# Kernel optimization log

Measured on AMD Instinct MI355X. Metric: run time of the kernel, lower is better.

Reference implementation:

```python
import jax, jax.numpy as jnp
import numpy as np

FEATURE_DIM = 128
HIDDEN_DIM = 64
MAPPING_SIZE = 64
SCALE = 10.0
B, N, H, W = 8, 65536, 56, 56


def setup_inputs() -> dict:
    key = jax.random.key(0)
    ks = jax.random.split(key, 12)
    features = jax.random.normal(ks[0], (B, FEATURE_DIM, H, W), dtype=jnp.float32)
    # points in [-1, 1]^3
    points = jax.random.uniform(ks[1], (B, N, 3), dtype=jnp.float32, minval=-1.0, maxval=1.0)
    # realistic pinhole intrinsics for a 56x56 feature map
    k_mat = jnp.array([[56.0, 0.0, 28.0], [0.0, 56.0, 28.0], [0.0, 0.0, 1.0]], dtype=jnp.float32)
    k = jnp.broadcast_to(k_mat, (B, 3, 3))
    # extrinsics: identity rotation, translate z by 2 so points are in front of camera
    rt_mat = jnp.concatenate([jnp.eye(3, dtype=jnp.float32), jnp.array([[0.0], [0.0], [2.0]], dtype=jnp.float32)], axis=1)
    rt = jnp.broadcast_to(rt_mat, (B, 3, 4))
    # learned params
    B_gauss = jax.random.normal(ks[2], (MAPPING_SIZE, 3), dtype=jnp.float32) * SCALE
    input_dim = FEATURE_DIM + 2 * MAPPING_SIZE
    W1 = jax.random.normal(ks[3], (input_dim, HIDDEN_DIM), dtype=jnp.float32) * 0.05
    b1 = jnp.zeros((HIDDEN_DIM,), dtype=jnp.float32)
    W2 = jax.random.normal(ks[4], (HIDDEN_DIM, HIDDEN_DIM), dtype=jnp.float32) * 0.05
    b2 = jnp.zeros((HIDDEN_DIM,), dtype=jnp.float32)
    W3 = jax.random.normal(ks[5], (HIDDEN_DIM, HIDDEN_DIM), dtype=jnp.float32) * 0.05
    b3 = jnp.zeros((HIDDEN_DIM,), dtype=jnp.float32)
    W4 = jax.random.normal(ks[6], (HIDDEN_DIM, 1), dtype=jnp.float32) * 0.05
    b4 = jnp.zeros((1,), dtype=jnp.float32)
    return {"features": features, "points": points, "k": k, "rt": rt,
            "B_gauss": B_gauss, "W1": W1, "b1": b1, "W2": W2, "b2": b2,
            "W3": W3, "b3": b3, "W4": W4, "b4": b4}


def _grid_sample_bilinear_zeros(grid, x, y):
    # grid: (B, C, H, W); x, y: (B, N) pixel coords (align_corners=False already unnormalized)
    Bc, C, Hc, Wc = grid.shape
    g = jnp.transpose(grid, (0, 2, 3, 1))  # (B, H, W, C)
    x0 = jnp.floor(x)
    y0 = jnp.floor(y)
    wx1 = x - x0  # frac
    wy1 = y - y0
    wx0 = 1.0 - wx1
    wy0 = 1.0 - wy1
    x0i = x0.astype(jnp.int32)
    y0i = y0.astype(jnp.int32)
    bidx = jnp.arange(Bc, dtype=jnp.int32)[:, None]  # (B, 1)

    def gather(ix, iy):
        inb = ((ix >= 0) & (ix < Wc) & (iy >= 0) & (iy < Hc)).astype(grid.dtype)  # (B, N)
        vals = g[bidx, jnp.clip(iy, 0, Hc - 1), jnp.clip(ix, 0, Wc - 1)]  # (B, N, C)
        return vals * inb[..., None]

    out = (gather(x0i, y0i) * (wx0 * wy0)[..., None]
           + gather(x0i + 1, y0i) * (wx1 * wy0)[..., None]
           + gather(x0i, y0i + 1) * (wx0 * wy1)[..., None]
           + gather(x0i + 1, y0i + 1) * (wx1 * wy1)[..., None])
    return out  # (B, N, C)


def reference(features, points, k, rt, B_gauss, W1, b1, W2, b2, W3, b3, W4, b4):
    Bc, Nc, _ = points.shape
    Hc, Wc = features.shape[-2:]
    # --- camera projection ---
    homo = jnp.concatenate([points, jnp.ones((Bc, Nc, 1), dtype=points.dtype)], axis=2)  # (B,N,4)
    cam = jnp.einsum('bij,bnj->bni', rt, homo)   # (B,N,3)
    img = jnp.einsum('bij,bnj->bni', k, cam)     # (B,N,3)
    z = img[:, :, 2:3] + 1e-8
    uv = img[:, :, :2] / z
    valid = (img[:, :, 2:3] > 0).astype(points.dtype)  # (B,N,1)
    u_norm = (2.0 * uv[..., 0] + 1.0) / Wc - 1.0
    v_norm = (2.0 * uv[..., 1] + 1.0) / Hc - 1.0
    # grid_sample align_corners=False unnormalization: ix = ((g+1)*W - 1)/2
    x = ((u_norm + 1.0) * Wc - 1.0) * 0.5
    y = ((v_norm + 1.0) * Hc - 1.0) * 0.5
    img_feats = _grid_sample_bilinear_zeros(features, x, y) * valid  # (B,N,C)
    # --- Fourier mapping ---
    x_proj = (2.0 * np.pi) * jnp.einsum('bnd,md->bnm', points, B_gauss)  # (B,N,M)
    coord_feats = jnp.concatenate([jnp.sin(x_proj), jnp.cos(x_proj)], axis=-1)  # (B,N,2M)
    # --- MLP ---
    inp = jnp.concatenate([img_feats, coord_feats], axis=2)  # (B,N,C+2M)
    h = jax.nn.relu(inp @ W1 + b1)
    h = jax.nn.relu(h @ W2 + b2)
    h = jax.nn.relu(h @ W3 + b3)
    out = h @ W4 + b4  # (B,N,1)
    return out
```

## Files before the change

### kernel.cpp

```cpp
#include <hip/hip_runtime.h>

#define FDIM 128
#define HDIM 64
#define MSIZE 64
#define IMG_W 56
#define IMG_H 56
#define NPIX (IMG_W * IMG_H)
#define NB 8
#define NPTS 65536

typedef _Float16 f16x8 __attribute__((ext_vector_type(8)));
typedef __fp16 hf16x2 __attribute__((ext_vector_type(2)));
typedef float f32x4 __attribute__((ext_vector_type(4)));

#define W2_OFF 16384
#define W3_OFF 20480
#define BG_OFF 49152
#define FT_BYTE_OFF 50176
#define TR16_BLOCKS (NPIX / 16 * NB)

__device__ __forceinline__ void lds_fence() {
    __asm__ volatile("s_waitcnt lgkmcnt(0)" ::: "memory");
}

__global__ __launch_bounds__(256) void prep_kernel(const float* __restrict__ in,
                                                   const float* __restrict__ W1,
                                                   const float* __restrict__ W2,
                                                   const float* __restrict__ W3,
                                                   const float* __restrict__ Bg,
                                                   _Float16* __restrict__ ws) {
    if (blockIdx.x < TR16_BLOCKS) {
        __shared__ float tile[16][133];
        _Float16* out = ws + FT_BYTE_OFF / 2;
        const int b = blockIdx.x / (NPIX / 16);
        const int pbase = (blockIdx.x % (NPIX / 16)) * 16;
        const int t = threadIdx.x;
        const float* src = in + (size_t)b * FDIM * NPIX;
        _Float16*    dst = out + (size_t)b * NPIX * FDIM;
        const int pq = t & 3;
        const int ch = t >> 2;
#pragma unroll
        for (int it = 0; it < 2; ++it) {
            const int c = it * 64 + ch;
            const float4 v = *(const float4*)(src + (size_t)c * NPIX + pbase + pq * 4);
            tile[pq * 4 + 0][c] = v.x;
            tile[pq * 4 + 1][c] = v.y;
            tile[pq * 4 + 2][c] = v.z;
            tile[pq * 4 + 3][c] = v.w;
        }
        __syncthreads();
        const int px = t >> 4;
        const int hk = (t & 15) * 8;
        union { f16x8 v; hf16x2 h[4]; } hv;
#pragma unroll
        for (int j = 0; j < 4; ++j)
            hv.h[j] = __builtin_amdgcn_cvt_pkrtz(tile[px][hk + 2 * j], tile[px][hk + 2 * j + 1]);
        *(f16x8*)(dst + (size_t)(pbase + px) * FDIM + hk) = hv.v;
    } else if (blockIdx.x < TR16_BLOCKS + 12) {
        const int t = (blockIdx.x - TR16_BLOCKS) * 256 + threadIdx.x;
        const int l = t & 63;
        const int q = l >> 4;
        const int col = l & 15;
        const int frag = t >> 6;
        if (frag < 32) {
            const int kt = frag >> 2, nt = frag & 3;
#pragma unroll
            for (int j = 0; j < 8; ++j) {
                int k = kt * 32 + q * 8 + j;
                int row = (k < 128) ? k : (128 + (k & 1) * 64 + ((k - 128) >> 1));
                ws[((size_t)(frag * 64 + l)) * 8 + j] = (_Float16)W1[row * HDIM + nt * 16 + col];
            }
        } else if (frag < 40) {
            const int f2 = frag - 32;
            const int kt = f2 >> 2, nt = f2 & 3;
#pragma unroll
            for (int j = 0; j < 8; ++j) {
                int row = kt * 32 + q * 8 + j;
                ws[W2_OFF + ((size_t)(f2 * 64 + l)) * 8 + j] = (_Float16)W2[row * HDIM + nt * 16 + col];
            }
        } else {
            const int f3 = frag - 40;
            const int kt = f3 >> 2, nt = f3 & 3;
#pragma unroll
            for (int j = 0; j < 8; ++j) {
                int row = kt * 32 + q * 8 + j;
                ws[W3_OFF + ((size_t)(f3 * 64 + l)) * 8 + j] = (_Float16)W3[row * HDIM + nt * 16 + col];
            }
        }
    } else {
        const int t = threadIdx.x;
        if (t < MSIZE) {
            float* bgs = (float*)((char*)ws + BG_OFF);
            bgs[t]       = Bg[t * 3 + 0];
            bgs[64 + t]  = Bg[t * 3 + 1];
            bgs[128 + t] = Bg[t * 3 + 2];
        }
    }
}

struct Rec {
    float w0[2], w1[2], w2[2], w3[2];
    int   i0[2], i1[2], i2[2], i3[2];
    float qx[2], qy[2], qz[2];
};
struct Pref {
    f16x8 a00, a10, a01, a11;
    f16x8 e00, e10, e01, e11;
};

__device__ __forceinline__ Pref pre_issue(const _Float16* __restrict__ ft,
                                          const Rec& R, int q) {
    Pref P;
    const int co0 = q * 8;
    P.a00 = *(const f16x8*)(ft + R.i0[0] + co0);
    P.a10 = *(const f16x8*)(ft + R.i1[0] + co0);
    P.a01 = *(const f16x8*)(ft + R.i2[0] + co0);
    P.a11 = *(const f16x8*)(ft + R.i3[0] + co0);
    const int co1 = 32 + q * 8;
    P.e00 = *(const f16x8*)(ft + R.i0[0] + co1);
    P.e10 = *(const f16x8*)(ft + R.i1[0] + co1);
    P.e01 = *(const f16x8*)(ft + R.i2[0] + co1);
    P.e11 = *(const f16x8*)(ft + R.i3[0] + co1);
    return P;
}

__device__ __forceinline__ void phaseF(f32x4 acc[2][4], const _Float16* __restrict__ w1l,
                                       const float* __restrict__ bgs, const Rec& R,
                                       int q, int l) {
#pragma unroll
    for (int ktf = 0; ktf < 4; ++ktf) {
        const f32x4 bgx = *(const f32x4*)(bgs + ktf * 16 + q * 4);
        const f32x4 bgy = *(const f32x4*)(bgs + 64 + ktf * 16 + q * 4);
        const f32x4 bgz = *(const f32x4*)(bgs + 128 + ktf * 16 + q * 4);
        f16x8 bf[4];
#pragma unroll
        for (int nt = 0; nt < 4; ++nt)
            bf[nt] = *(const f16x8*)(w1l + ((size_t)(((4 + ktf) * 4 + nt) * 64 + l)) * 8);
#pragma unroll
        for (int mt = 0; mt < 2; ++mt) {
            union { f16x8 v; hf16x2 h[4]; } af;
#pragma unroll
            for (int i = 0; i < 4; ++i) {
                float t = bgx[i] * R.qx[mt] + bgy[i] * R.qy[mt] + bgz[i] * R.qz[mt];
                float tf = __builtin_amdgcn_fractf(t);
                af.h[i] = __builtin_amdgcn_cvt_pkrtz(__builtin_amdgcn_sinf(tf),
                                                     __builtin_amdgcn_cosf(tf));
            }
#pragma unroll
            for (int nt = 0; nt < 4; ++nt)
                acc[mt][nt] = __builtin_amdgcn_mfma_f32_16x16x32_f16(af.v, bf[nt], acc[mt][nt], 0, 0, 0);
        }
    }
}

__device__ __forceinline__ void phaseI(f32x4 acc[2][4], const _Float16* __restrict__ ft,
                                       const _Float16* __restrict__ w1l, const Rec& R,
                                       Pref& P, int q, int l) {
    _Float16 wh[2][4];
#pragma unroll
    for (int mt = 0; mt < 2; ++mt) {
        wh[mt][0] = (_Float16)R.w0[mt]; wh[mt][1] = (_Float16)R.w1[mt];
        wh[mt][2] = (_Float16)R.w2[mt]; wh[mt][3] = (_Float16)R.w3[mt];
    }
#pragma unroll
    for (int s = 0; s < 8; ++s) {
        const int mt = s >> 2;
        f16x8 t00, t10, t01, t11;
        if (s < 6) {
            const int nmt = (s + 2) >> 2, nktg = (s + 2) & 3;
            const int co = nktg * 32 + q * 8;
            t00 = *(const f16x8*)(ft + R.i0[nmt] + co);
            t10 = *(const f16x8*)(ft + R.i1[nmt] + co);
            t01 = *(const f16x8*)(ft + R.i2[nmt] + co);
            t11 = *(const f16x8*)(ft + R.i3[nmt] + co);
        }
        f16x8 af = P.a00 * wh[mt][0] + P.a10 * wh[mt][1] + P.a01 * wh[mt][2] + P.a11 * wh[mt][3];
        const int ktg = s & 3;
#pragma unroll
        for (int nt = 0; nt < 4; ++nt) {
            f16x8 bf = *(const f16x8*)(w1l + ((size_t)((ktg * 4 + nt) * 64 + l)) * 8);
            acc[mt][nt] = __builtin_amdgcn_mfma_f32_16x16x32_f16(af, bf, acc[mt][nt], 0, 0, 0);
        }
        P.a00 = P.e00; P.a10 = P.e10; P.a01 = P.e01; P.a11 = P.e11;
        P.e00 = t00; P.e10 = t10; P.e01 = t01; P.e11 = t11;
    }
}

__device__ __forceinline__ void mlp_tail(f32x4 acc[2][4], _Float16* __restrict__ Ah,
                                         const _Float16* __restrict__ wfrag,
                                         const float* __restrict__ b1,
                                         const float* __restrict__ b2,
                                         const float* __restrict__ b3,
                                         const float* __restrict__ W4,
                                         const float* __restrict__ b4,
                                         float* __restrict__ out, int outbase,
                                         int q, int col, int l) {
    const f32x4 zero4 = {0.0f, 0.0f, 0.0f, 0.0f};
    f16x8 bfW[8];
#pragma unroll
    for (int f = 0; f < 8; ++f)
        bfW[f] = *(const f16x8*)(wfrag + W2_OFF + ((size_t)(f * 64 + l)) * 8);

    float bb[4];
#pragma unroll
    for (int nt = 0; nt < 4; ++nt) bb[nt] = b1[nt * 16 + col];
#pragma unroll
    for (int mt = 0; mt < 2; ++mt)
#pragma unroll
        for (int nt = 0; nt < 4; ++nt)
#pragma unroll
            for (int r = 0; r < 4; ++r) {
                float hv = fmaxf(acc[mt][nt][r] + bb[nt], 0.0f);
                Ah[(mt * 16 + q * 4 + r) * 72 + nt * 16 + col] = (_Float16)hv;
            }
    lds_fence();

#pragma unroll
    for (int mt = 0; mt < 2; ++mt)
#pragma unroll
        for (int nt = 0; nt < 4; ++nt) acc[mt][nt] = zero4;
#pragma unroll
    for (int ktl = 0; ktl < 2; ++ktl)
#pragma unroll
        for (int mt = 0; mt < 2; ++mt) {
            f16x8 af = *(const f16x8*)(&Ah[(mt * 16 + col) * 72 + ktl * 32 + q * 8]);
#pragma unroll
            for (int nt = 0; nt < 4; ++nt)
                acc[mt][nt] = __builtin_amdgcn_mfma_f32_16x16x32_f16(af, bfW[ktl * 4 + nt], acc[mt][nt], 0, 0, 0);
        }

#pragma unroll
    for (int f = 0; f < 8; ++f)
        bfW[f] = *(const f16x8*)(wfrag + W3_OFF + ((size_t)(f * 64 + l)) * 8);

    lds_fence();
#pragma unroll
    for (int nt = 0; nt < 4; ++nt) bb[nt] = b2[nt * 16 + col];
#pragma unroll
    for (int mt = 0; mt < 2; ++mt)
#pragma unroll
        for (int nt = 0; nt < 4; ++nt)
#pragma unroll
            for (int r = 0; r < 4; ++r) {
                float hv = fmaxf(acc[mt][nt][r] + bb[nt], 0.0f);
                Ah[(mt * 16 + q * 4 + r) * 72 + nt * 16 + col] = (_Float16)hv;
            }
    lds_fence();

#pragma unroll
    for (int mt = 0; mt < 2; ++mt)
#pragma unroll
        for (int nt = 0; nt < 4; ++nt) acc[mt][nt] = zero4;
#pragma unroll
    for (int ktl = 0; ktl < 2; ++ktl)
#pragma unroll
        for (int mt = 0; mt < 2; ++mt) {
            f16x8 af = *(const f16x8*)(&Ah[(mt * 16 + col) * 72 + ktl * 32 + q * 8]);
#pragma unroll
            for (int nt = 0; nt < 4; ++nt)
                acc[mt][nt] = __builtin_amdgcn_mfma_f32_16x16x32_f16(af, bfW[ktl * 4 + nt], acc[mt][nt], 0, 0, 0);
        }

    float b3v[4], w4v[4];
#pragma unroll
    for (int nt = 0; nt < 4; ++nt) {
        b3v[nt] = b3[nt * 16 + col];
        w4v[nt] = W4[nt * 16 + col];
    }
    const float b4v = b4[0];
#pragma unroll
    for (int mt = 0; mt < 2; ++mt)
#pragma unroll
        for (int r = 0; r < 4; ++r) {
            float p = 0.0f;
#pragma unroll
            for (int nt = 0; nt < 4; ++nt)
                p = fmaf(fmaxf(acc[mt][nt][r] + b3v[nt], 0.0f), w4v[nt], p);
            p += __shfl_xor(p, 1);
            p += __shfl_xor(p, 2);
            p += __shfl_xor(p, 4);
            p += __shfl_xor(p, 8);
            if (col == 0) out[outbase + mt * 16 + q * 4 + r] = p + b4v;
        }
    lds_fence();
}

__global__ __launch_bounds__(256, 3) void decoder_mfma7(
    const _Float16* __restrict__ ft,
    const float* __restrict__ points,
    const float* __restrict__ Kmat, const float* __restrict__ Rt,
    const _Float16* __restrict__ wfrag,
    const float* __restrict__ b1, const float* __restrict__ b2,
    const float* __restrict__ b3,
    const float* __restrict__ W4, const float* __restrict__ b4,
    float* __restrict__ out) {
    __shared__ _Float16 w1l[16384];
    __shared__ _Float16 lds[4 * 32 * 72];
    const int tid = threadIdx.x;
    const int wid = tid >> 6;
    const int l   = tid & 63;
    const int q   = l >> 4;
    const int col = l & 15;
    const int b     = blockIdx.x & 7;
    const int grp   = blockIdx.x >> 3;
    const int wbase = b * NPTS + grp * 256 + wid * 64;
    _Float16* Ah = lds + wid * 32 * 72;
    const float* bgs = (const float*)((const char*)wfrag + BG_OFF);

#pragma unroll
    for (int i = 0; i < 8; ++i)
        ((f16x8*)w1l)[i * 256 + tid] = ((const f16x8*)wfrag)[i * 256 + tid];

    const int gid = wbase + l;
    const float px = points[(size_t)gid * 3 + 0];
    const float py = points[(size_t)gid * 3 + 1];
    const float pz = points[(size_t)gid * 3 + 2];
    const float* rt = Rt + b * 12;
    const float* km = Kmat + b * 9;
    float cx = rt[0] * px + rt[1] * py + rt[2]  * pz + rt[3];
    float cy = rt[4] * px + rt[5] * py + rt[6]  * pz + rt[7];
    float cz = rt[8] * px + rt[9] * py + rt[10] * pz + rt[11];
    float ix = km[0] * cx + km[1] * cy + km[2] * cz;
    float iy = km[3] * cx + km[4] * cy + km[5] * cz;
    float iz = km[6] * cx + km[7] * cy + km[8] * cz;
    float z  = iz + 1e-8f;
    float u  = ix / z;
    float v  = iy / z;
    float valid = (iz > 0.0f) ? 1.0f : 0.0f;
    float u_norm = (2.0f * u + 1.0f) / (float)IMG_W - 1.0f;
    float v_norm = (2.0f * v + 1.0f) / (float)IMG_H - 1.0f;
    float x = ((u_norm + 1.0f) * (float)IMG_W - 1.0f) * 0.5f;
    float y = ((v_norm + 1.0f) * (float)IMG_H - 1.0f) * 0.5f;
    float x0f = floorf(x), y0f = floorf(y);
    float wx1 = x - x0f, wy1 = y - y0f;
    float wx0 = 1.0f - wx1, wy0 = 1.0f - wy1;
    int x0 = (int)x0f, y0 = (int)y0f;
    int x1 = x0 + 1, y1 = y0 + 1;
    int x0c = x0 < 0 ? 0 : (x0 > IMG_W - 1 ? IMG_W - 1 : x0);
    int x1c = x1 < 0 ? 0 : (x1 > IMG_W - 1 ? IMG_W - 1 : x1);
    int y0c = y0 < 0 ? 0 : (y0 > IMG_H - 1 ? IMG_H - 1 : y0);
    int y1c = y1 < 0 ? 0 : (y1 > IMG_H - 1 ? IMG_H - 1 : y1);
    float mx0 = (x0 >= 0 && x0 < IMG_W) ? 1.0f : 0.0f;
    float mx1 = (x1 >= 0 && x1 < IMG_W) ? 1.0f : 0.0f;
    float my0 = (y0 >= 0 && y0 < IMG_H) ? 1.0f : 0.0f;
    float my1 = (y1 >= 0 && y1 < IMG_H) ? 1.0f : 0.0f;
    const int pb = b * NPIX;
    float r_w00 = wx0 * wy0 * mx0 * my0 * valid;
    float r_w10 = wx1 * wy0 * mx1 * my0 * valid;
    float r_w01 = wx0 * wy1 * mx0 * my1 * valid;
    float r_w11 = wx1 * wy1 * mx1 * my1 * valid;
    int r_i00 = (pb + y0c * IMG_W + x0c) * FDIM;
    int r_i10 = (pb + y0c * IMG_W + x1c) * FDIM;
    int r_i01 = (pb + y1c * IMG_W + x0c) * FDIM;
    int r_i11 = (pb + y1c * IMG_W + x1c) * FDIM;

    f32x4 acc[2][4];
    const f32x4 zero4 = {0.0f, 0.0f, 0.0f, 0.0f};

    {
        Rec R0;
#pragma unroll
        for (int mt = 0; mt < 2; ++mt) {
            const int src = mt * 16 + col;
            R0.w0[mt] = __shfl(r_w00, src);
            R0.w1[mt] = __shfl(r_w10, src);
            R0.w2[mt] = __shfl(r_w01, src);
            R0.w3[mt] = __shfl(r_w11, src);
            R0.i0[mt] = __shfl(r_i00, src);
            R0.i1[mt] = __shfl(r_i10, src);
            R0.i2[mt] = __shfl(r_i01, src);
            R0.i3[mt] = __shfl(r_i11, src);
            R0.qx[mt] = __shfl(px, src);
            R0.qy[mt] = __shfl(py, src);
            R0.qz[mt] = __shfl(pz, src);
        }
        Pref P0 = pre_issue(ft, R0, q);
        __syncthreads();
#pragma unroll
        for (int mt = 0; mt < 2; ++mt)
#pragma unroll
            for (int nt = 0; nt < 4; ++nt) acc[mt][nt] = zero4;
        phaseF(acc, w1l, bgs, R0, q, l);
        phaseI(acc, ft, w1l, R0, P0, q, l);
        mlp_tail(acc, Ah, wfrag, b1, b2, b3, W4, b4, out, wbase, q, col, l);
    }

    __builtin_amdgcn_sched_barrier(0);

    {
        Rec R1;
#pragma unroll
        for (int mt = 0; mt < 2; ++mt) {
            const int src = 32 + mt * 16 + col;
            R1.w0[mt] = __shfl(r_w00, src);
            R1.w1[mt] = __shfl(r_w10, src);
            R1.w2[mt] = __shfl(r_w01, src);
            R1.w3[mt] = __shfl(r_w11, src);
            R1.i0[mt] = __shfl(r_i00, src);
            R1.i1[mt] = __shfl(r_i10, src);
            R1.i2[mt] = __shfl(r_i01, src);
            R1.i3[mt] = __shfl(r_i11, src);
            R1.qx[mt] = __shfl(px, src);
            R1.qy[mt] = __shfl(py, src);
            R1.qz[mt] = __shfl(pz, src);
        }
        Pref P1 = pre_issue(ft, R1, q);
#pragma unroll
        for (int mt = 0; mt < 2; ++mt)
#pragma unroll
            for (int nt = 0; nt < 4; ++nt) acc[mt][nt] = zero4;
        phaseF(acc, w1l, bgs, R1, q, l);
        phaseI(acc, ft, w1l, R1, P1, q, l);
        mlp_tail(acc, Ah, wfrag, b1, b2, b3, W4, b4, out, wbase + 32, q, col, l);
    }
}

__global__ __launch_bounds__(64, 2) void decoder_valu(
    const float* __restrict__ feats, const float* __restrict__ points,
    const float* __restrict__ Kmat, const float* __restrict__ Rt,
    const float* __restrict__ Bg,
    const float* __restrict__ W1, const float* __restrict__ b1,
    const float* __restrict__ W2, const float* __restrict__ b2,
    const float* __restrict__ W3, const float* __restrict__ b3,
    const float* __restrict__ W4, const float* __restrict__ b4,
    float* __restrict__ out) {
    __shared__ float hbuf[64 * 65];
    const int tid = threadIdx.x;
    const int b   = blockIdx.x / (NPTS / 64);
    const int gid = blockIdx.x * 64 + tid;
    const float px = points[(size_t)gid * 3 + 0];
    const float py = points[(size_t)gid * 3 + 1];
    const float pz = points[(size_t)gid * 3 + 2];
    const float* rt = Rt + b * 12;
    const float* km = Kmat + b * 9;
    float cx = rt[0] * px + rt[1] * py + rt[2]  * pz + rt[3];
    float cy = rt[4] * px + rt[5] * py + rt[6]  * pz + rt[7];
    float cz = rt[8] * px + rt[9] * py + rt[10] * pz + rt[11];
    float ix = km[0] * cx + km[1] * cy + km[2] * cz;
    float iy = km[3] * cx + km[4] * cy + km[5] * cz;
    float iz = km[6] * cx + km[7] * cy + km[8] * cz;
    float z  = iz + 1e-8f;
    float u  = ix / z, v = iy / z;
    float valid = (iz > 0.0f) ? 1.0f : 0.0f;
    float u_norm = (2.0f * u + 1.0f) / (float)IMG_W - 1.0f;
    float v_norm = (2.0f * v + 1.0f) / (float)IMG_H - 1.0f;
    float x = ((u_norm + 1.0f) * (float)IMG_W - 1.0f) * 0.5f;
    float y = ((v_norm + 1.0f) * (float)IMG_H - 1.0f) * 0.5f;
    float x0f = floorf(x), y0f = floorf(y);
    float wx1 = x - x0f, wy1 = y - y0f;
    float wx0 = 1.0f - wx1, wy0 = 1.0f - wy1;
    int x0 = (int)x0f, y0 = (int)y0f;
    int x1 = x0 + 1, y1 = y0 + 1;
    int x0c = x0 < 0 ? 0 : (x0 > IMG_W - 1 ? IMG_W - 1 : x0);
    int x1c = x1 < 0 ? 0 : (x1 > IMG_W - 1 ? IMG_W - 1 : x1);
    int y0c = y0 < 0 ? 0 : (y0 > IMG_H - 1 ? IMG_H - 1 : y0);
    int y1c = y1 < 0 ? 0 : (y1 > IMG_H - 1 ? IMG_H - 1 : y1);
    float mx0 = (x0 >= 0 && x0 < IMG_W) ? 1.0f : 0.0f;
    float mx1 = (x1 >= 0 && x1 < IMG_W) ? 1.0f : 0.0f;
    float my0 = (y0 >= 0 && y0 < IMG_H) ? 1.0f : 0.0f;
    float my1 = (y1 >= 0 && y1 < IMG_H) ? 1.0f : 0.0f;
    float w00 = wx0 * wy0 * mx0 * my0 * valid;
    float w10 = wx1 * wy0 * mx1 * my0 * valid;
    float w01 = wx0 * wy1 * mx0 * my1 * valid;
    float w11 = wx1 * wy1 * mx1 * my1 * valid;
    float h[HDIM];
#pragma unroll
    for (int j = 0; j < HDIM; ++j) h[j] = b1[j];
    const float* fb = feats + (size_t)b * FDIM * NPIX;
    const int p00 = y0c * IMG_W + x0c, p10 = y0c * IMG_W + x1c;
    const int p01 = y1c * IMG_W + x0c, p11 = y1c * IMG_W + x1c;
#pragma unroll 1
    for (int c = 0; c < FDIM; ++c) {
        const float* fp = fb + (size_t)c * NPIX;
        float fv = w00 * fp[p00] + w10 * fp[p10] + w01 * fp[p01] + w11 * fp[p11];
        const float* wr = W1 + (size_t)c * HDIM;
#pragma unroll
        for (int j = 0; j < HDIM; ++j) h[j] = fmaf(fv, wr[j], h[j]);
    }
#pragma unroll 1
    for (int m = 0; m < MSIZE; ++m) {
        float t = Bg[m * 3 + 0] * px + Bg[m * 3 + 1] * py + Bg[m * 3 + 2] * pz;
        float tf = t - floorf(t);
        float s = __builtin_amdgcn_sinf(tf);
        float c = __builtin_amdgcn_cosf(tf);
        const float* wsn = W1 + (size_t)(FDIM + m) * HDIM;
        const float* wcs = W1 + (size_t)(FDIM + MSIZE + m) * HDIM;
#pragma unroll
        for (int j = 0; j < HDIM; ++j)
            h[j] = fmaf(s, wsn[j], fmaf(c, wcs[j], h[j]));
    }
    float* myh = &hbuf[tid * 65];
#pragma unroll
    for (int j = 0; j < HDIM; ++j) myh[j] = fmaxf(h[j], 0.0f);
    float h2[HDIM];
#pragma unroll
    for (int j = 0; j < HDIM; ++j) h2[j] = b2[j];
#pragma unroll 1
    for (int i = 0; i < HDIM; ++i) {
        float hi = myh[i];
        const float* wr = W2 + (size_t)i * HDIM;
#pragma unroll
        for (int j = 0; j < HDIM; ++j) h2[j] = fmaf(hi, wr[j], h2[j]);
    }
#pragma unroll
    for (int j = 0; j < HDIM; ++j) myh[j] = fmaxf(h2[j], 0.0f);
#pragma unroll
    for (int j = 0; j < HDIM; ++j) h[j] = b3[j];
#pragma unroll 1
    for (int i = 0; i < HDIM; ++i) {
        float hi = myh[i];
        const float* wr = W3 + (size_t)i * HDIM;
#pragma unroll
        for (int j = 0; j < HDIM; ++j) h[j] = fmaf(hi, wr[j], h[j]);
    }
    float acc = b4[0];
#pragma unroll
    for (int j = 0; j < HDIM; ++j) acc = fmaf(fmaxf(h[j], 0.0f), W4[j], acc);
    out[gid] = acc;
}

extern "C" void kernel_launch(void* const* d_in, const int* in_sizes, int n_in,
                              void* d_out, int out_size, void* d_ws, size_t ws_size,
                              hipStream_t stream) {
    const float* feats = (const float*)d_in[0];
    const float* pts   = (const float*)d_in[1];
    const float* k     = (const float*)d_in[2];
    const float* rt    = (const float*)d_in[3];
    const float* Bg    = (const float*)d_in[4];
    const float* W1    = (const float*)d_in[5];
    const float* b1    = (const float*)d_in[6];
    const float* W2    = (const float*)d_in[7];
    const float* b2    = (const float*)d_in[8];
    const float* W3    = (const float*)d_in[9];
    const float* b3    = (const float*)d_in[10];
    const float* W4    = (const float*)d_in[11];
    const float* b4    = (const float*)d_in[12];
    float* out = (float*)d_out;

    const size_t ftBytes = (size_t)NB * NPIX * FDIM * sizeof(_Float16);

    if (ws_size >= FT_BYTE_OFF + ftBytes) {
        _Float16* wf = (_Float16*)d_ws;
        _Float16* ft = (_Float16*)((char*)d_ws + FT_BYTE_OFF);
        prep_kernel<<<TR16_BLOCKS + 13, 256, 0, stream>>>(feats, W1, W2, W3, Bg, wf);
        decoder_mfma7<<<NB * NPTS / 256, 256, 0, stream>>>(ft, pts, k, rt, wf,
                                                           b1, b2, b3, W4, b4, out);
    } else {
        decoder_valu<<<NB * NPTS / 64, 64, 0, stream>>>(feats, pts, k, rt, Bg,
                                                        W1, b1, W2, b2, W3, b3, W4, b4, out);
    }
}
```

Before: 170.8 us.

## Precompute feature-map projection through W1 before bilinear sampling

Bilinear interpolation is linear, so the change first multiplies the 8x3136 feature map by the image half of W1 with a new GEMM kernel, giving a 64-wide projected map G. The decoder then gathers and blends four 64-wide G rows per point instead of four 128-wide feature rows, and adds the result to the Fourier-term accumulator before the layer-1 ReLU. This halves the gathered bytes per point and removes 524k points' worth of 128-K MFMA work, at the cost of an extra kernel launch and a G buffer round trip. The image part of layer 1 is now also added after fp16 rounding, which changes numerics slightly.

```diff
diff --git a/kernel.cpp b/kernel.cpp
--- a/kernel.cpp
+++ b/kernel.cpp
@@ -17,6 +17,7 @@
 #define W3_OFF 20480
 #define BG_OFF 49152
 #define FT_BYTE_OFF 50176
+#define G_BYTE_OFF 6472704
 #define TR16_BLOCKS (NPIX / 16 * NB)
 
 __device__ __forceinline__ void lds_fence() {
@@ -98,31 +99,54 @@
     }
 }
 
+__global__ __launch_bounds__(256, 4) void gemm_g(_Float16* __restrict__ ws) {
+    const int tid = threadIdx.x;
+    const int wid = tid >> 6;
+    const int l   = tid & 63;
+    const int q   = l >> 4;
+    const int col = l & 15;
+    const int T = blockIdx.x * 4 + wid;
+    const int b = T / (NPIX / 32);
+    const int tile = T % (NPIX / 32);
+    const int pbase = tile * 32;
+    const _Float16* ft = ws + FT_BYTE_OFF / 2;
+    _Float16* Gp = ws + G_BYTE_OFF / 2;
+    const f32x4 zero4 = {0.0f, 0.0f, 0.0f, 0.0f};
+    f32x4 acc[2][4];
+#pragma unroll
+    for (int mt = 0; mt < 2; ++mt)
+#pragma unroll
+        for (int nt = 0; nt < 4; ++nt) acc[mt][nt] = zero4;
+#pragma unroll
+    for (int kt = 0; kt < 4; ++kt) {
+        f16x8 bf[4];
+#pragma unroll
+        for (int nt = 0; nt < 4; ++nt)
+            bf[nt] = *(const f16x8*)(ws + ((size_t)((kt * 4 + nt) * 64 + l)) * 8);
+#pragma unroll
+        for (int mt = 0; mt < 2; ++mt) {
+            f16x8 af = *(const f16x8*)(ft + ((size_t)(b * NPIX + pbase + mt * 16 + col)) * FDIM
+                                       + kt * 32 + q * 8);
+#pragma unroll
+            for (int nt = 0; nt < 4; ++nt)
+                acc[mt][nt] = __builtin_amdgcn_mfma_f32_16x16x32_f16(af, bf[nt], acc[mt][nt], 0, 0, 0);
+        }
+    }
+#pragma unroll
+    for (int mt = 0; mt < 2; ++mt)
+#pragma unroll
+        for (int nt = 0; nt < 4; ++nt)
+#pragma unroll
+            for (int r = 0; r < 4; ++r)
+                Gp[((size_t)(b * NPIX + pbase + mt * 16 + q * 4 + r)) * HDIM + nt * 16 + col]
+                    = (_Float16)acc[mt][nt][r];
+}
+
 struct Rec {
     float w0[2], w1[2], w2[2], w3[2];
     int   i0[2], i1[2], i2[2], i3[2];
     float qx[2], qy[2], qz[2];
 };
-struct Pref {
-    f16x8 a00, a10, a01, a11;
-    f16x8 e00, e10, e01, e11;
-};
-
-__device__ __forceinline__ Pref pre_issue(const _Float16* __restrict__ ft,
-                                          const Rec& R, int q) {
-    Pref P;
-    const int co0 = q * 8;
-    P.a00 = *(const f16x8*)(ft + R.i0[0] + co0);
-    P.a10 = *(const f16x8*)(ft + R.i1[0] + co0);
-    P.a01 = *(const f16x8*)(ft + R.i2[0] + co0);
-    P.a11 = *(const f16x8*)(ft + R.i3[0] + co0);
-    const int co1 = 32 + q * 8;
-    P.e00 = *(const f16x8*)(ft + R.i0[0] + co1);
-    P.e10 = *(const f16x8*)(ft + R.i1[0] + co1);
-    P.e01 = *(const f16x8*)(ft + R.i2[0] + co1);
-    P.e11 = *(const f16x8*)(ft + R.i3[0] + co1);
-    return P;
-}
 
 __device__ __forceinline__ void phaseF(f32x4 acc[2][4], const _Float16* __restrict__ w1l,
                                        const float* __restrict__ bgs, const Rec& R,
@@ -135,7 +159,7 @@
         f16x8 bf[4];
 #pragma unroll
         for (int nt = 0; nt < 4; ++nt)
-            bf[nt] = *(const f16x8*)(w1l + ((size_t)(((4 + ktf) * 4 + nt) * 64 + l)) * 8);
+            bf[nt] = *(const f16x8*)(w1l + ((size_t)((ktf * 4 + nt) * 64 + l)) * 8);
 #pragma unroll
         for (int mt = 0; mt < 2; ++mt) {
             union { f16x8 v; hf16x2 h[4]; } af;
@@ -153,53 +177,40 @@
     }
 }
 
-__device__ __forceinline__ void phaseI(f32x4 acc[2][4], const _Float16* __restrict__ ft,
-                                       const _Float16* __restrict__ w1l, const Rec& R,
-                                       Pref& P, int q, int l) {
+__device__ __forceinline__ void mlp_tail2(f32x4 acc[2][4], _Float16* __restrict__ Ah,
+                                          const _Float16* __restrict__ wfrag,
+                                          const _Float16* __restrict__ Gp,
+                                          const Rec& R,
+                                          const float* __restrict__ b1,
+                                          const float* __restrict__ b2,
+                                          const float* __restrict__ b3,
+                                          const float* __restrict__ W4,
+                                          const float* __restrict__ b4,
+                                          float* __restrict__ out, int outbase,
+                                          int q, int col, int l) {
+    const f32x4 zero4 = {0.0f, 0.0f, 0.0f, 0.0f};
+    f16x8 g[2][2][4];
+#pragma unroll
+    for (int ktl = 0; ktl < 2; ++ktl)
+#pragma unroll
+        for (int mt = 0; mt < 2; ++mt) {
+            const int co = ktl * 32 + q * 8;
+            g[ktl][mt][0] = *(const f16x8*)(Gp + R.i0[mt] + co);
+            g[ktl][mt][1] = *(const f16x8*)(Gp + R.i1[mt] + co);
+            g[ktl][mt][2] = *(const f16x8*)(Gp + R.i2[mt] + co);
+            g[ktl][mt][3] = *(const f16x8*)(Gp + R.i3[mt] + co);
+        }
+    f16x8 bfW[8];
+#pragma unroll
+    for (int f = 0; f < 8; ++f)
+        bfW[f] = *(const f16x8*)(wfrag + W2_OFF + ((size_t)(f * 64 + l)) * 8);
+
     _Float16 wh[2][4];
 #pragma unroll
     for (int mt = 0; mt < 2; ++mt) {
         wh[mt][0] = (_Float16)R.w0[mt]; wh[mt][1] = (_Float16)R.w1[mt];
         wh[mt][2] = (_Float16)R.w2[mt]; wh[mt][3] = (_Float16)R.w3[mt];
     }
-#pragma unroll
-    for (int s = 0; s < 8; ++s) {
-        const int mt = s >> 2;
-        f16x8 t00, t10, t01, t11;
-        if (s < 6) {
-            const int nmt = (s + 2) >> 2, nktg = (s + 2) & 3;
-            const int co = nktg * 32 + q * 8;
-            t00 = *(const f16x8*)(ft + R.i0[nmt] + co);
-            t10 = *(const f16x8*)(ft + R.i1[nmt] + co);
-            t01 = *(const f16x8*)(ft + R.i2[nmt] + co);
-            t11 = *(const f16x8*)(ft + R.i3[nmt] + co);
-        }
-        f16x8 af = P.a00 * wh[mt][0] + P.a10 * wh[mt][1] + P.a01 * wh[mt][2] + P.a11 * wh[mt][3];
-        const int ktg = s & 3;
-#pragma unroll
-        for (int nt = 0; nt < 4; ++nt) {
-            f16x8 bf = *(const f16x8*)(w1l + ((size_t)((ktg * 4 + nt) * 64 + l)) * 8);
-            acc[mt][nt] = __builtin_amdgcn_mfma_f32_16x16x32_f16(af, bf, acc[mt][nt], 0, 0, 0);
-        }
-        P.a00 = P.e00; P.a10 = P.e10; P.a01 = P.e01; P.a11 = P.e11;
-        P.e00 = t00; P.e10 = t10; P.e01 = t01; P.e11 = t11;
-    }
-}
-
-__device__ __forceinline__ void mlp_tail(f32x4 acc[2][4], _Float16* __restrict__ Ah,
-                                         const _Float16* __restrict__ wfrag,
-                                         const float* __restrict__ b1,
-                                         const float* __restrict__ b2,
-                                         const float* __restrict__ b3,
-                                         const float* __restrict__ W4,
-                                         const float* __restrict__ b4,
-                                         float* __restrict__ out, int outbase,
-                                         int q, int col, int l) {
-    const f32x4 zero4 = {0.0f, 0.0f, 0.0f, 0.0f};
-    f16x8 bfW[8];
-#pragma unroll
-    for (int f = 0; f < 8; ++f)
-        bfW[f] = *(const f16x8*)(wfrag + W2_OFF + ((size_t)(f * 64 + l)) * 8);
 
     float bb[4];
 #pragma unroll
@@ -209,10 +220,9 @@
 #pragma unroll
         for (int nt = 0; nt < 4; ++nt)
 #pragma unroll
-            for (int r = 0; r < 4; ++r) {
-                float hv = fmaxf(acc[mt][nt][r] + bb[nt], 0.0f);
-                Ah[(mt * 16 + q * 4 + r) * 72 + nt * 16 + col] = (_Float16)hv;
-            }
+            for (int r = 0; r < 4; ++r)
+                Ah[(mt * 16 + q * 4 + r) * 72 + nt * 16 + col]
+                    = (_Float16)(acc[mt][nt][r] + bb[nt]);
     lds_fence();
 
 #pragma unroll
@@ -224,6 +234,11 @@
 #pragma unroll
         for (int mt = 0; mt < 2; ++mt) {
             f16x8 af = *(const f16x8*)(&Ah[(mt * 16 + col) * 72 + ktl * 32 + q * 8]);
+            af = af + g[ktl][mt][0] * wh[mt][0] + g[ktl][mt][1] * wh[mt][1]
+                    + g[ktl][mt][2] * wh[mt][2] + g[ktl][mt][3] * wh[mt][3];
+#pragma unroll
+            for (int j = 0; j < 8; ++j)
+                af[j] = af[j] > (_Float16)0.0f ? af[j] : (_Float16)0.0f;
 #pragma unroll
             for (int nt = 0; nt < 4; ++nt)
                 acc[mt][nt] = __builtin_amdgcn_mfma_f32_16x16x32_f16(af, bfW[ktl * 4 + nt], acc[mt][nt], 0, 0, 0);
@@ -285,8 +300,8 @@
     lds_fence();
 }
 
-__global__ __launch_bounds__(256, 3) void decoder_mfma7(
-    const _Float16* __restrict__ ft,
+__global__ __launch_bounds__(256, 3) void decoder_mfma8(
+    const _Float16* __restrict__ Gp,
     const float* __restrict__ points,
     const float* __restrict__ Kmat, const float* __restrict__ Rt,
     const _Float16* __restrict__ wfrag,
@@ -294,7 +309,7 @@
     const float* __restrict__ b3,
     const float* __restrict__ W4, const float* __restrict__ b4,
     float* __restrict__ out) {
-    __shared__ _Float16 w1l[16384];
+    __shared__ _Float16 w1l[8192];
     __shared__ _Float16 lds[4 * 32 * 72];
     const int tid = threadIdx.x;
     const int wid = tid >> 6;
@@ -308,8 +323,8 @@
     const float* bgs = (const float*)((const char*)wfrag + BG_OFF);
 
 #pragma unroll
-    for (int i = 0; i < 8; ++i)
-        ((f16x8*)w1l)[i * 256 + tid] = ((const f16x8*)wfrag)[i * 256 + tid];
+    for (int i = 0; i < 4; ++i)
+        ((f16x8*)w1l)[i * 256 + tid] = ((const f16x8*)(wfrag + 8192))[i * 256 + tid];
 
     const int gid = wbase + l;
     const float px = points[(size_t)gid * 3 + 0];
@@ -349,10 +364,10 @@
     float r_w10 = wx1 * wy0 * mx1 * my0 * valid;
     float r_w01 = wx0 * wy1 * mx0 * my1 * valid;
     float r_w11 = wx1 * wy1 * mx1 * my1 * valid;
-    int r_i00 = (pb + y0c * IMG_W + x0c) * FDIM;
-    int r_i10 = (pb + y0c * IMG_W + x1c) * FDIM;
-    int r_i01 = (pb + y1c * IMG_W + x0c) * FDIM;
-    int r_i11 = (pb + y1c * IMG_W + x1c) * FDIM;
+    int r_i00 = (pb + y0c * IMG_W + x0c) * HDIM;
+    int r_i10 = (pb + y0c * IMG_W + x1c) * HDIM;
+    int r_i01 = (pb + y1c * IMG_W + x0c) * HDIM;
+    int r_i11 = (pb + y1c * IMG_W + x1c) * HDIM;
 
     f32x4 acc[2][4];
     const f32x4 zero4 = {0.0f, 0.0f, 0.0f, 0.0f};
@@ -374,15 +389,13 @@
             R0.qy[mt] = __shfl(py, src);
             R0.qz[mt] = __shfl(pz, src);
         }
-        Pref P0 = pre_issue(ft, R0, q);
         __syncthreads();
 #pragma unroll
         for (int mt = 0; mt < 2; ++mt)
 #pragma unroll
             for (int nt = 0; nt < 4; ++nt) acc[mt][nt] = zero4;
         phaseF(acc, w1l, bgs, R0, q, l);
-        phaseI(acc, ft, w1l, R0, P0, q, l);
-        mlp_tail(acc, Ah, wfrag, b1, b2, b3, W4, b4, out, wbase, q, col, l);
+        mlp_tail2(acc, Ah, wfrag, Gp, R0, b1, b2, b3, W4, b4, out, wbase, q, col, l);
     }
 
     __builtin_amdgcn_sched_barrier(0);
@@ -404,14 +417,12 @@
             R1.qy[mt] = __shfl(py, src);
             R1.qz[mt] = __shfl(pz, src);
         }
-        Pref P1 = pre_issue(ft, R1, q);
 #pragma unroll
         for (int mt = 0; mt < 2; ++mt)
 #pragma unroll
             for (int nt = 0; nt < 4; ++nt) acc[mt][nt] = zero4;
         phaseF(acc, w1l, bgs, R1, q, l);
-        phaseI(acc, ft, w1l, R1, P1, q, l);
-        mlp_tail(acc, Ah, wfrag, b1, b2, b3, W4, b4, out, wbase + 32, q, col, l);
+        mlp_tail2(acc, Ah, wfrag, Gp, R1, b1, b2, b3, W4, b4, out, wbase + 32, q, col, l);
     }
 }
 
@@ -537,13 +548,15 @@
     const float* b4    = (const float*)d_in[12];
     float* out = (float*)d_out;
 
-    const size_t ftBytes = (size_t)NB * NPIX * FDIM * sizeof(_Float16);
-
-    if (ws_size >= FT_BYTE_OFF + ftBytes) {
+    const size_t gBytes = (size_t)NB * NPIX * HDIM * sizeof(_Float16);
+    const size_t need = G_BYTE_OFF + gBytes;
+
+    if (ws_size >= need) {
         _Float16* wf = (_Float16*)d_ws;
-        _Float16* ft = (_Float16*)((char*)d_ws + FT_BYTE_OFF);
+        _Float16* Gp = (_Float16*)((char*)d_ws + G_BYTE_OFF);
         prep_kernel<<<TR16_BLOCKS + 13, 256, 0, stream>>>(feats, W1, W2, W3, Bg, wf);
-        decoder_mfma7<<<NB * NPTS / 256, 256, 0, stream>>>(ft, pts, k, rt, wf,
+        gemm_g<<<NB * NPIX / 32 / 4, 256, 0, stream>>>(wf);
+        decoder_mfma8<<<NB * NPTS / 256, 256, 0, stream>>>(Gp, pts, k, rt, wf,
                                                            b1, b2, b3, W4, b4, out);
     } else {
         decoder_valu<<<NB * NPTS / 64, 64, 0, stream>>>(feats, pts, k, rt, Bg,
```

After: 151.8 us. 1.13x faster.
